# Performance work log

Hardware: AMD Instinct MI355X
Metric: run time of the kernel (lower is better)

## Reference

```python
import jax, jax.numpy as jnp
import numpy as np

N = 2000   # nodes
K = 16     # receptive-field size (exact degree incl. self-loop)
C_IN = 16  # input_feats
H = 16     # hidden_size
NC = 18    # num_contractions


def setup_inputs() -> dict:
    key = jax.random.key(0)
    k1, k2, k3, k4, k5, k6 = jax.random.split(key, 6)
    # adjacency with exactly K ones per row (self-loop + K-1 distinct random nbrs)
    u = jax.random.uniform(k1, (N, N))
    u = u.at[jnp.arange(N), jnp.arange(N)].set(-1.0)  # force self into top-K
    nbrs = jnp.argsort(u, axis=1)[:, :K]
    adj = jnp.zeros((N, N), jnp.float32).at[jnp.arange(N)[:, None], nbrs].set(1.0)
    X = jax.random.normal(k2, (N, C_IN), jnp.float32)
    scale = 0.1
    W1 = scale * jax.random.normal(k3, (H, NC * C_IN), jnp.float32)
    b1 = jnp.zeros((H,), jnp.float32)
    W2 = scale * jax.random.normal(k4, (H, NC * H), jnp.float32)
    b2 = jnp.zeros((H,), jnp.float32)
    fc_w = scale * jax.random.normal(k5, (1, 2 * H + C_IN), jnp.float32)
    fc_b = scale * jax.random.normal(k6, (1,), jnp.float32)
    return {"X": X, "adj": adj, "W1": W1, "b1": b1, "W2": W2, "b2": b2,
            "fc_w": fc_w, "fc_b": fc_b}


def _neighbors(adj):
    # each row has exactly K ones -> top_k returns their indices
    _, idx = jax.lax.top_k(adj, K)
    return jnp.sort(idx, axis=1)  # (N, K)


def _contract18(T):
    # T: (n, m, a, b, c) stacked promoted neighbor tensors; 18 contractions 3rd->2nd order
    n, k, _, _, c = T.shape
    tr = lambda M: jnp.swapaxes(M, 1, 2)
    s0, s1, s2 = T.sum(1), T.sum(2), T.sum(3)           # single-index sums
    d0 = jnp.einsum('ixxbc->ixbc', T)                    # diag m=a
    d1 = jnp.einsum('ixaxc->ixac', T)                    # diag m=b
    d2 = jnp.einsum('imyyc->imyc', T)                    # diag a=b
    outs = []
    for M in (s0, s1, s2, d0, d1, d2):
        outs.append(M)
        outs.append(tr(M))                               # 12 so far
    v0, v1, v2 = T.sum((2, 3)), T.sum((1, 3)), T.sum((1, 2))  # double sums -> vectors
    for v in (v0, v1, v2):
        outs.append(jnp.broadcast_to(v[:, :, None, :], (n, k, k, c)))  # rows
        outs.append(jnp.broadcast_to(v[:, None, :, :], (n, k, k, c)))  # cols
    return jnp.concatenate(outs, axis=-1)                # (n, k, k, 18c)


def _forward(X, adj, W1, b1, W2, b2, fc_w, fc_b):
    nbrs = _neighbors(adj)                               # (N, K)
    nbrs_nb = nbrs[nbrs]                                 # (N, K, K)
    # chi[i,m,a,b] = 1 iff a-th member of P_i equals b-th member of P_{nbrs[i,m]}
    chi = (nbrs[:, None, :, None] == nbrs_nb[:, :, None, :]).astype(X.dtype)  # (N,K,K,K)
    # F0: first->second order promotion (features on the diagonal of P_i x P_i)
    F0 = jnp.einsum('ab,iac->iabc', jnp.eye(K, dtype=X.dtype), X[nbrs])  # (N,K,K,C_IN)

    def step(F, W, b):
        Fn = F[nbrs]                                     # (N, m, p, q, c)
        tmp = jnp.einsum('imap,impqc->imaqc', chi, Fn)
        T = jnp.einsum('imaqc,imbq->imabc', tmp, chi)    # promoted + stacked (N,m,a,b,c)
        C = _contract18(T)                               # (N, a, b, 18c)
        return jax.nn.relu(jnp.einsum('iabk,hk->iabh', C, W) + b)

    F1 = step(F0, W1, b1)
    F2 = step(F1, W2, b2)
    g = jnp.concatenate([F0.sum((0, 1, 2)), F1.sum((0, 1, 2)), F2.sum((0, 1, 2))])
    return g @ fc_w.T + fc_b                             # (n_outputs,)


def reference(X, adj, W1, b1, W2, b2, fc_w, fc_b):
    return _forward(X, adj, W1, b1, W2, b2, fc_w, fc_b)
```

## Files before the change

### kernel.cpp

```cpp
#include <hip/hip_runtime.h>

#define NN 2000

typedef _Float16 halfx8 __attribute__((ext_vector_type(8)));
typedef float floatx4 __attribute__((ext_vector_type(4)));

#define LBAR() asm volatile("s_waitcnt lgkmcnt(0)\n\ts_barrier" ::: "memory")

__global__ void build_nbrs_k(const float* __restrict__ adj,
                             int* __restrict__ nbrs) {
    int i = blockIdx.x;
    int lane = threadIdx.x;
    const float* row = adj + (size_t)i * NN;
    float v[32];
#pragma unroll
    for (int c = 0; c < 32; ++c) {
        int col = c * 64 + lane;
        v[c] = (col < NN) ? row[col] : 0.0f;
    }
    int base = 0;
#pragma unroll
    for (int c = 0; c < 32; ++c) {
        bool p = v[c] > 0.5f;
        unsigned long long mask = __ballot(p);
        if (p) {
            int pos = base + __popcll(mask & ((1ull << lane) - 1ull));
            nbrs[i * 16 + pos] = c * 64 + lane;
        }
        base += __popcll(mask);
    }
}

__global__ void build_map_k(const int* __restrict__ nbrs,
                            signed char* __restrict__ map8,
                            signed char* __restrict__ imp8,
                            int4* __restrict__ aux) {
    int idx = blockIdx.x * blockDim.x + threadIdx.x;
    if (idx >= NN * 16) return;
    int i = idx >> 4;
    int m = idx & 15;
    int j = nbrs[idx];
    const int4* pi = (const int4*)(nbrs + (size_t)i * 16);
    const int4* pj = (const int4*)(nbrs + (size_t)j * 16);
    int4 A = pi[0], Bq = pi[1], C = pi[2], D = pi[3];
    int4 E = pj[0], F = pj[1], G = pj[2], H = pj[3];
    int ni[16] = {A.x,A.y,A.z,A.w, Bq.x,Bq.y,Bq.z,Bq.w, C.x,C.y,C.z,C.w, D.x,D.y,D.z,D.w};
    int nj[16] = {E.x,E.y,E.z,E.w, F.x,F.y,F.z,F.w, G.x,G.y,G.z,G.w, H.x,H.y,H.z,H.w};

    int mp[16];
    unsigned long long lo = 0, hi = 0;
#pragma unroll
    for (int a = 0; a < 16; ++a) {
        int r = -1;
#pragma unroll
        for (int p = 0; p < 16; ++p)
            if (nj[p] == ni[a]) r = p;
        mp[a] = r;
        unsigned long long b = (unsigned long long)(r & 0xff);
        if (a < 8) lo |= b << (8 * a); else hi |= b << (8 * (a - 8));
    }
    uint4 pk;
    pk.x = (unsigned)lo; pk.y = (unsigned)(lo >> 32);
    pk.z = (unsigned)hi; pk.w = (unsigned)(hi >> 32);
    *(uint4*)(map8 + ((size_t)idx << 4)) = pk;
    lo = 0; hi = 0;
#pragma unroll
    for (int p = 0; p < 16; ++p) {
        int r = -1;
#pragma unroll
        for (int a = 0; a < 16; ++a)
            if (ni[a] == nj[p]) r = a;
        unsigned long long b = (unsigned long long)(r & 0xff);
        if (p < 8) lo |= b << (8 * p); else hi |= b << (8 * (p - 8));
    }
    pk.x = (unsigned)lo; pk.y = (unsigned)(lo >> 32);
    pk.z = (unsigned)hi; pk.w = (unsigned)(hi >> 32);
    *(uint4*)(imp8 + ((size_t)idx << 4)) = pk;

    unsigned vm = 0;
    int a1 = -1, a2 = -1, pa1 = 0, pa2 = 0;
#pragma unroll
    for (int a = 0; a < 16; ++a) {
        if (mp[a] >= 0) {
            vm |= (1u << a);
            if (a1 < 0)      { a1 = a; pa1 = mp[a]; }
            else if (a2 < 0) { a2 = a; pa2 = mp[a]; }
        }
    }
    int ms = 0;
#pragma unroll
    for (int a = 0; a < 16; ++a)
        if (ni[a] == i) ms = a;
    int4 av;
    av.x = j;
    av.y = (a1 & 0xff) | ((pa1 & 0xff) << 8) | ((a2 & 0xff) << 16) | ((pa2 & 0xff) << 24);
    av.z = (int)(vm | ((unsigned)(mp[m] & 0xff) << 16) | ((unsigned)(ms & 0xff) << 24));
    av.w = 0;
    aux[idx] = av;
}

__global__ void prep_w_k(const float* __restrict__ W1,
                         const float* __restrict__ W2,
                         _Float16* __restrict__ Wpk) {
    int idx = blockIdx.x * blockDim.x + threadIdx.x;
    if (idx >= 2 * 10 * 512) return;
    int stage = idx / 5120;
    int rem = idx % 5120;
    int chunk = rem / 512;
    int r2 = rem % 512;
    int L = r2 / 8, jj = r2 % 8;
    int q = L >> 4, h = L & 15;
    int k = q * 8 + jj;
    const int tA[10] = {2, 6, 10, 0, 14,   3, 7, 11, 1, 15};
    const int tB[10] = {4, 8, -1, 12, 16,  5, 9, -1, 13, 17};
    int tblk = (k < 16) ? tA[chunk] : tB[chunk];
    int c = k & 15;
    const float* W = stage ? W2 : W1;
    float val = (tblk < 0) ? 0.f : W[h * 288 + tblk * 16 + c];
    Wpk[idx] = (_Float16)val;
}

template <int DIAG>
__global__ __launch_bounds__(256, 2)
void step_k(const float* __restrict__ Fp,
            const float* __restrict__ Xp,
            const _Float16* __restrict__ Wpk,
            const float* __restrict__ bias,
            const signed char* __restrict__ map8,
            const signed char* __restrict__ imp8,
            const int4* __restrict__ auxp,
            float* __restrict__ Fout,
            float* __restrict__ gp0,
            float* __restrict__ gp) {
    __shared__ __attribute__((aligned(16))) float S0[16][16][18];
    __shared__ __attribute__((aligned(16))) _Float16 MAP[5][16][16][16];
    __shared__ __attribute__((aligned(16))) float V0f[16][16];
    __shared__ __attribute__((aligned(16))) float V1f[16][16];
    __shared__ __attribute__((aligned(16))) float V2f[16][16];
    __shared__ __attribute__((aligned(16))) float S1f[16][16];

    const int i = blockIdx.x;
    const int t = threadIdx.x;
    const int u = t >> 4;
    const int l = t & 15;
    const int lane = t & 63, q = lane >> 4, h = lane & 15, wv = t >> 6;

    int4 av = auxp[i * 16 + u];
    uint4 imv = *(const uint4*)(imp8 + ((size_t)(i * 16 + u) << 4));
    float bv = bias[l];
    const int j = av.x;
    const int a1 = (int)(signed char)(av.y & 0xff);
    const int pa1 = (av.y >> 8) & 0xff;
    const int a2 = (int)(signed char)((av.y >> 16) & 0xff);
    const int pa2 = (av.y >> 24) & 0xff;
    const unsigned vm = (unsigned)(av.z & 0xffff);
    const int pmm = (av.z >> 16) & 0xff;
    const int ms = (av.z >> 24) & 0xff;

    float frow[16], fcol[16], xv = 0.f;
    if (DIAG) {
        xv = Xp[(size_t)j * 16 + l];
    } else {
        const float* Fi = Fp + (size_t)i * 4096;
#pragma unroll
        for (int b = 0; b < 16; ++b) frow[b] = Fi[(u * 16 + b) * 16 + l];
#pragma unroll
        for (int a = 0; a < 16; ++a) fcol[a] = Fi[(a * 16 + u) * 16 + l];
    }

    float R1[16], R2[16];
    if (!DIAG && u != ms) {
        const float* P1 = Fp + (((size_t)j * 256 + pa1 * 16) * 16) + l;
#pragma unroll
        for (int p = 0; p < 16; ++p) R1[p] = P1[p * 16];
        if (a2 >= 0) {
            const float* P2 = Fp + (((size_t)j * 256 + pa2 * 16) * 16) + l;
#pragma unroll
            for (int p = 0; p < 16; ++p) R2[p] = P2[p * 16];
        }
    }
    halfx8 Bf[10];
    {
        const halfx8* Wp8 = (const halfx8*)Wpk;
#pragma unroll
        for (int c = 0; c < 10; ++c) Bf[c] = Wp8[c * 64 + lane];
    }

    if (u != ms) {
        uint4 z = {0u, 0u, 0u, 0u};
#pragma unroll
        for (int k = 0; k < 5; ++k) {
            *(uint4*)&MAP[k][u][l][0] = z;
            *(uint4*)&MAP[k][u][l][8] = z;
        }
    }
    if (DIAG) {
        S1f[u][l] = xv;
        V1f[u][l] = xv;
        V2f[u][l] = xv;
#pragma unroll
        for (int b = 0; b < 16; ++b) S0[u][b][l] = (b == u) ? xv : 0.f;
        MAP[0][ms][u][l] = (_Float16)xv;
        MAP[1][ms][u][l] = (_Float16)xv;
        _Float16 dz = (_Float16)((u == ms) ? xv : 0.f);
        MAP[2][ms][u][l] = dz;
        MAP[3][ms][u][l] = dz;
        MAP[4][ms][u][l] = (_Float16)xv;
    } else {
        float s2 = 0.f, a10 = 0.f, a8 = 0.f;
#pragma unroll
        for (int b = 0; b < 16; ++b) {
            float v = frow[b];
            s2 += v;
            S0[u][b][l] = v;
            if (b == u)  a10 = v;
            if (b == ms) a8 = v;
        }
        float s1 = 0.f, a6 = 0.f;
#pragma unroll
        for (int a = 0; a < 16; ++a) {
            float v = fcol[a];
            s1 += v;
            if (a == ms) a6 = v;
        }
        S1f[u][l] = s2;
        V1f[u][l] = s2;
        V2f[u][l] = s1;
        MAP[0][ms][u][l] = (_Float16)s1;
        MAP[1][ms][u][l] = (_Float16)s2;
        MAP[2][ms][u][l] = (_Float16)a6;
        MAP[3][ms][u][l] = (_Float16)a8;
        MAP[4][ms][u][l] = (_Float16)a10;
    }
    LBAR();

    if (u != ms) {
        const int m = u;
        float v0acc = 0.f;
        if (DIAG) {
#pragma unroll
            for (int a = 0; a < 16; ++a) {
                if ((vm >> a) & 1u) {
                    float v = S1f[a][l];
                    v0acc += v;
                    atomicAdd(&S0[a][a][l], v);
                    atomicAdd(&V1f[a][l], v);
                    atomicAdd(&V2f[a][l], v);
                    MAP[0][m][a][l] = (_Float16)v;
                    MAP[1][m][a][l] = (_Float16)v;
                    MAP[4][m][a][l] = (_Float16)v;
                    if (a == m) { MAP[2][m][m][l] = (_Float16)v; MAP[3][m][m][l] = (_Float16)v; }
                }
            }
        } else {
            float colacc[16];
#pragma unroll
            for (int p = 0; p < 16; ++p) colacc[p] = 0.f;
            auto process = [&](int a, int pa, const float (&vr)[16]) {
                float rowacc = 0.f, a8v = 0.f, a10v = 0.f;
                const bool am = (a == m);
#pragma unroll
                for (int p = 0; p < 16; ++p) {
                    float v = vr[p];
                    if (p == pmm) a8v = v;
                    if (p == pa)  a10v = v;
                    unsigned dw = (p < 4) ? imv.x : ((p < 8) ? imv.y : ((p < 12) ? imv.z : imv.w));
                    int b = (int)(signed char)((dw >> (8 * (p & 3))) & 0xffu);
                    if (b >= 0) {
                        rowacc += v;
                        colacc[p] += v;
                        atomicAdd(&S0[a][b][l], v);
                        atomicAdd(&V2f[b][l], v);
                        if (am) MAP[2][m][b][l] = (_Float16)v;
                    }
                }
                v0acc += rowacc;
                atomicAdd(&V1f[a][l], rowacc);
                MAP[1][m][a][l] = (_Float16)rowacc;
                MAP[3][m][a][l] = (_Float16)a8v;
                MAP[4][m][a][l] = (_Float16)a10v;
            };
            process(a1, pa1, R1);
            if (a2 >= 0) process(a2, pa2, R2);
            unsigned rm = vm & ~(1u << a1);
            if (a2 >= 0) rm &= ~(1u << a2);
            if (rm) {
                uint4 mpq = *(const uint4*)(map8 + ((size_t)(i * 16 + u) << 4));
                do {
                    int a = __builtin_ctz(rm); rm &= rm - 1;
                    unsigned dw = (a & 8) ? ((a & 4) ? mpq.w : mpq.z) : ((a & 4) ? mpq.y : mpq.x);
                    int pa = (int)(signed char)((dw >> (8 * (a & 3))) & 0xffu);
                    float RT[16];
                    const float* P3 = Fp + (((size_t)j * 256 + pa * 16) * 16) + l;
#pragma unroll
                    for (int p = 0; p < 16; ++p) RT[p] = P3[p * 16];
                    process(a, pa, RT);
                } while (rm);
            }
#pragma unroll
            for (int p = 0; p < 16; ++p) {
                unsigned dw = (p < 4) ? imv.x : ((p < 8) ? imv.y : ((p < 12) ? imv.z : imv.w));
                int b = (int)(signed char)((dw >> (8 * (p & 3))) & 0xffu);
                if (b >= 0) MAP[0][m][b][l] = (_Float16)colacc[p];
            }
        }
        V0f[m][l] = v0acc;
    } else {
        float v0s = 0.f;
#pragma unroll
        for (int b = 0; b < 16; ++b) v0s += S1f[b][l];
        V0f[ms][l] = v0s;
        if (DIAG) gp0[l * 2048 + i] = v0s;
    }

    floatx4 acc1[4], acc2[4];
#pragma unroll
    for (int tt = 0; tt < 4; ++tt) {
        acc1[tt] = (floatx4){0.f, 0.f, 0.f, 0.f};
        acc2[tt] = (floatx4){0.f, 0.f, 0.f, 0.f};
    }
    halfx8 az;
#pragma unroll
    for (int z = 0; z < 8; ++z) az[z] = (_Float16)0.f;
    const int wbase = wv * 4;
#pragma unroll
    for (int tt = 0; tt < 4; ++tt) {
        const int x = wbase + tt;
        halfx8 p0, p1, p2;
        if (q < 2) {
            p0 = *(const halfx8*)&MAP[0][x][h][q * 8];
            p1 = *(const halfx8*)&MAP[2][x][h][q * 8];
            p2 = *(const halfx8*)&MAP[4][x][h][q * 8];
        } else {
            const int c0 = (q - 2) * 8;
            p0 = *(const halfx8*)&MAP[1][x][h][c0];
            p1 = *(const halfx8*)&MAP[3][x][h][c0];
            p2 = az;
        }
        acc1[tt] = __builtin_amdgcn_mfma_f32_16x16x32_f16(p0, Bf[0], acc1[tt], 0, 0, 0);
        acc1[tt] = __builtin_amdgcn_mfma_f32_16x16x32_f16(p1, Bf[1], acc1[tt], 0, 0, 0);
        acc1[tt] = __builtin_amdgcn_mfma_f32_16x16x32_f16(p2, Bf[2], acc1[tt], 0, 0, 0);
        acc2[tt] = __builtin_amdgcn_mfma_f32_16x16x32_f16(p0, Bf[5], acc2[tt], 0, 0, 0);
        acc2[tt] = __builtin_amdgcn_mfma_f32_16x16x32_f16(p1, Bf[6], acc2[tt], 0, 0, 0);
        acc2[tt] = __builtin_amdgcn_mfma_f32_16x16x32_f16(p2, Bf[7], acc2[tt], 0, 0, 0);
    }
    LBAR();

    auto cvt8 = [](const float* p) -> halfx8 {
        float2 fa = *(const float2*)p, fb = *(const float2*)(p + 2),
               fc = *(const float2*)(p + 4), fd = *(const float2*)(p + 6);
        halfx8 r;
        r[0] = (_Float16)fa.x; r[1] = (_Float16)fa.y; r[2] = (_Float16)fb.x; r[3] = (_Float16)fb.y;
        r[4] = (_Float16)fc.x; r[5] = (_Float16)fc.y; r[6] = (_Float16)fd.x; r[7] = (_Float16)fd.y;
        return r;
    };
    auto cvt8a = [](const float* p) -> halfx8 {
        float4 va = *(const float4*)p, vb = *(const float4*)(p + 4);
        halfx8 r;
        r[0] = (_Float16)va.x; r[1] = (_Float16)va.y; r[2] = (_Float16)va.z; r[3] = (_Float16)va.w;
        r[4] = (_Float16)vb.x; r[5] = (_Float16)vb.y; r[6] = (_Float16)vb.z; r[7] = (_Float16)vb.w;
        return r;
    };
#pragma unroll
    for (int tt = 0; tt < 4; ++tt) {
        const int x = wbase + tt;
        halfx8 p3, p4;
        if (q < 2) {
            p3 = cvt8(&S0[x][h][q * 8]);
            p4 = cvt8a(&V1f[x][q * 8]);
        } else {
            const int c0 = (q - 2) * 8;
            p3 = cvt8a(&V0f[x][c0]);
            p4 = cvt8a(&V2f[x][c0]);
        }
        acc1[tt] = __builtin_amdgcn_mfma_f32_16x16x32_f16(p3, Bf[3], acc1[tt], 0, 0, 0);
        acc1[tt] = __builtin_amdgcn_mfma_f32_16x16x32_f16(p4, Bf[4], acc1[tt], 0, 0, 0);
        acc2[tt] = __builtin_amdgcn_mfma_f32_16x16x32_f16(p3, Bf[8], acc2[tt], 0, 0, 0);
        acc2[tt] = __builtin_amdgcn_mfma_f32_16x16x32_f16(p4, Bf[9], acc2[tt], 0, 0, 0);
    }

    float* P2f = (float*)&MAP[0][0][0][0];
#pragma unroll
    for (int tt = 0; tt < 4; ++tt) {
        const int x = wbase + tt;
#pragma unroll
        for (int r = 0; r < 4; ++r)
            P2f[(x * 16 + (q * 4 + r)) * 17 + h] = acc2[tt][r];
    }
    LBAR();

    float gpart = 0.f;
#pragma unroll
    for (int tt = 0; tt < 4; ++tt) {
        const int x = wbase + tt;
#pragma unroll
        for (int r = 0; r < 4; ++r) {
            const int y = q * 4 + r;
            float val = acc1[tt][r] + P2f[(y * 16 + x) * 17 + h] + bv;
            val = fmaxf(val, 0.f);
            gpart += val;
            if (Fout) Fout[(size_t)i * 4096 + (x * 16 + y) * 16 + h] = val;
        }
    }
    gpart += __shfl_xor(gpart, 16, 64);
    gpart += __shfl_xor(gpart, 32, 64);
    if (lane < 16) gp[h * 8192 + i * 4 + wv] = gpart;
}

__global__ void reduce_g_k(const float* __restrict__ parts,
                           float* __restrict__ gsum) {
    int r = blockIdx.x;
    const float* p;
    int cnt4;
    if (r < 16)      { p = parts + r * 2048;                    cnt4 = 500;  }
    else if (r < 32) { p = parts + 32768 + (r - 16) * 8192;     cnt4 = 2000; }
    else             { p = parts + 163840 + (r - 32) * 8192;    cnt4 = 2000; }
    const float4* p4 = (const float4*)p;
    int t = threadIdx.x;
    float s = 0.f;
    for (int n = t; n < cnt4; n += 256) {
        float4 v = p4[n];
        s += v.x + v.y + v.z + v.w;
    }
#pragma unroll
    for (int off = 32; off > 0; off >>= 1) s += __shfl_xor(s, off, 64);
    __shared__ float wsum[4];
    if ((t & 63) == 0) wsum[t >> 6] = s;
    __syncthreads();
    if (t == 0) gsum[r] = wsum[0] + wsum[1] + wsum[2] + wsum[3];
}

__global__ void finalize_k(const float* __restrict__ gsum,
                           const float* __restrict__ fcw,
                           const float* __restrict__ fcb,
                           float* __restrict__ out) {
    int t = threadIdx.x;
    float v = (t < 48) ? gsum[t] * fcw[t] : 0.f;
#pragma unroll
    for (int off = 32; off > 0; off >>= 1) v += __shfl_xor(v, off, 64);
    if (t == 0) out[0] = v + fcb[0];
}

extern "C" void kernel_launch(void* const* d_in, const int* in_sizes, int n_in,
                              void* d_out, int out_size, void* d_ws, size_t ws_size,
                              hipStream_t stream) {
    const float* X   = (const float*)d_in[0];
    const float* adj = (const float*)d_in[1];
    const float* W1  = (const float*)d_in[2];
    const float* b1  = (const float*)d_in[3];
    const float* W2  = (const float*)d_in[4];
    const float* b2  = (const float*)d_in[5];
    const float* fcw = (const float*)d_in[6];
    const float* fcb = (const float*)d_in[7];
    float* out = (float*)d_out;
    char* ws = (char*)d_ws;

    float*       gsum  = (float*)(ws + 0);
    int*         nbrs  = (int*)(ws + 1024);
    signed char* map8  = (signed char*)(ws + 129280);
    signed char* imp8  = (signed char*)(ws + 641280);
    int4*        aux   = (int4*)(ws + 1153280);
    float*       parts = (float*)(ws + 1665280);
    _Float16*    Wpk   = (_Float16*)(ws + 2844928);
    float*       F1    = (float*)(ws + 2865408);

    build_nbrs_k<<<NN, 64, 0, stream>>>(adj, nbrs);
    build_map_k<<<(NN * 16 + 255) / 256, 256, 0, stream>>>(nbrs, map8, imp8, aux);
    prep_w_k<<<40, 256, 0, stream>>>(W1, W2, Wpk);
    step_k<1><<<NN, 256, 0, stream>>>(nullptr, X, Wpk, b1, map8, imp8, aux, F1,
                                      parts, parts + 32768);
    step_k<0><<<NN, 256, 0, stream>>>(F1, X, Wpk + 5120, b2, map8, imp8, aux, nullptr,
                                      nullptr, parts + 163840);
    reduce_g_k<<<48, 256, 0, stream>>>(parts, gsum);
    finalize_k<<<1, 64, 0, stream>>>(gsum, fcw, fcb, out);
}
```

Measured before the change: 158.1 us.

## Store MAP contraction tiles in FP8 and use FP8 MFMA for them

The five MAP contraction planes are now stored in shared memory as FP8 bytes, and the matching weight chunks are packed as FP8. The first group of matmuls uses fp8 MFMA instructions, while the S0/V-vector path stays in FP16. This halves the LDS footprint of MAP and drops the S0 padding, so launch bounds can rise from 2 to 4 blocks per CU for more occupancy. The cost is reduced precision on those contraction terms, plus extra conversion instructions, and possibly more LDS bank conflicts from the unpadded S0 atomics.

```diff
diff --git a/kernel.cpp b/kernel.cpp
--- a/kernel.cpp
+++ b/kernel.cpp
@@ -6,6 +6,10 @@
 typedef float floatx4 __attribute__((ext_vector_type(4)));
 
 #define LBAR() asm volatile("s_waitcnt lgkmcnt(0)\n\ts_barrier" ::: "memory")
+
+__device__ __forceinline__ unsigned char to_fp8(float v) {
+    return (unsigned char)(__builtin_amdgcn_cvt_pk_fp8_f32(v, 0.f, 0, false) & 0xff);
+}
 
 __global__ void build_nbrs_k(const float* __restrict__ adj,
                              int* __restrict__ nbrs) {
@@ -101,30 +105,50 @@
 
 __global__ void prep_w_k(const float* __restrict__ W1,
                          const float* __restrict__ W2,
-                         _Float16* __restrict__ Wpk) {
+                         unsigned char* __restrict__ Wpk8,
+                         _Float16* __restrict__ Wpk16) {
     int idx = blockIdx.x * blockDim.x + threadIdx.x;
-    if (idx >= 2 * 10 * 512) return;
-    int stage = idx / 5120;
-    int rem = idx % 5120;
-    int chunk = rem / 512;
-    int r2 = rem % 512;
-    int L = r2 / 8, jj = r2 % 8;
-    int q = L >> 4, h = L & 15;
-    int k = q * 8 + jj;
-    const int tA[10] = {2, 6, 10, 0, 14,   3, 7, 11, 1, 15};
-    const int tB[10] = {4, 8, -1, 12, 16,  5, 9, -1, 13, 17};
-    int tblk = (k < 16) ? tA[chunk] : tB[chunk];
-    int c = k & 15;
-    const float* W = stage ? W2 : W1;
-    float val = (tblk < 0) ? 0.f : W[h * 288 + tblk * 16 + c];
-    Wpk[idx] = (_Float16)val;
+    if (idx >= 10240) return;
+    if (idx < 6144) {
+        int stage = idx / 3072;
+        int r = idx % 3072;
+        int c = r / 512;
+        int r2 = r % 512;
+        int L = r2 >> 3, jj = r2 & 7;
+        int q = L >> 4, h = L & 15;
+        int k = q * 8 + jj;
+        const int bA[6] = {2, 6, 10, 3, 7, 11};
+        const int bB[6] = {4, 8, -1, 5, 9, -1};
+        int tb = (k < 16) ? bA[c] : bB[c];
+        int ci = k & 15;
+        const float* W = stage ? W2 : W1;
+        float val = (tb < 0) ? 0.f : W[h * 288 + tb * 16 + ci];
+        Wpk8[idx] = to_fp8(val);
+    } else {
+        int id2 = idx - 6144;
+        int stage = id2 / 2048;
+        int r = id2 % 2048;
+        int c = r / 512;
+        int r2 = r % 512;
+        int L = r2 >> 3, jj = r2 & 7;
+        int q = L >> 4, h = L & 15;
+        int k = q * 8 + jj;
+        const int bA[4] = {0, 14, 1, 15};
+        const int bB[4] = {12, 16, 13, 17};
+        int tb = (k < 16) ? bA[c] : bB[c];
+        int ci = k & 15;
+        const float* W = stage ? W2 : W1;
+        float val = W[h * 288 + tb * 16 + ci];
+        Wpk16[id2] = (_Float16)val;
+    }
 }
 
 template <int DIAG>
-__global__ __launch_bounds__(256, 2)
+__global__ __launch_bounds__(256, 4)
 void step_k(const float* __restrict__ Fp,
             const float* __restrict__ Xp,
-            const _Float16* __restrict__ Wpk,
+            const unsigned char* __restrict__ Wpk8s,
+            const _Float16* __restrict__ Wpk16s,
             const float* __restrict__ bias,
             const signed char* __restrict__ map8,
             const signed char* __restrict__ imp8,
@@ -132,8 +156,8 @@
             float* __restrict__ Fout,
             float* __restrict__ gp0,
             float* __restrict__ gp) {
-    __shared__ __attribute__((aligned(16))) float S0[16][16][18];
-    __shared__ __attribute__((aligned(16))) _Float16 MAP[5][16][16][16];
+    __shared__ __attribute__((aligned(16))) float S0[16][16][16];
+    __shared__ __attribute__((aligned(16))) unsigned char MAP8[5][16][16][16];
     __shared__ __attribute__((aligned(16))) float V0f[16][16];
     __shared__ __attribute__((aligned(16))) float V1f[16][16];
     __shared__ __attribute__((aligned(16))) float V2f[16][16];
@@ -179,20 +203,24 @@
             for (int p = 0; p < 16; ++p) R2[p] = P2[p * 16];
         }
     }
-    halfx8 Bf[10];
+    long Bf8[6];
     {
-        const halfx8* Wp8 = (const halfx8*)Wpk;
-#pragma unroll
-        for (int c = 0; c < 10; ++c) Bf[c] = Wp8[c * 64 + lane];
+        const long* Wq8 = (const long*)Wpk8s;
+#pragma unroll
+        for (int c = 0; c < 6; ++c) Bf8[c] = Wq8[c * 64 + lane];
+    }
+    halfx8 Bf16[4];
+    {
+        const halfx8* Wq16 = (const halfx8*)Wpk16s;
+#pragma unroll
+        for (int c = 0; c < 4; ++c) Bf16[c] = Wq16[c * 64 + lane];
     }
 
     if (u != ms) {
         uint4 z = {0u, 0u, 0u, 0u};
 #pragma unroll
-        for (int k = 0; k < 5; ++k) {
-            *(uint4*)&MAP[k][u][l][0] = z;
-            *(uint4*)&MAP[k][u][l][8] = z;
-        }
+        for (int k = 0; k < 5; ++k)
+            *(uint4*)&MAP8[k][u][l][0] = z;
     }
     if (DIAG) {
         S1f[u][l] = xv;
@@ -200,12 +228,13 @@
         V2f[u][l] = xv;
 #pragma unroll
         for (int b = 0; b < 16; ++b) S0[u][b][l] = (b == u) ? xv : 0.f;
-        MAP[0][ms][u][l] = (_Float16)xv;
-        MAP[1][ms][u][l] = (_Float16)xv;
-        _Float16 dz = (_Float16)((u == ms) ? xv : 0.f);
-        MAP[2][ms][u][l] = dz;
-        MAP[3][ms][u][l] = dz;
-        MAP[4][ms][u][l] = (_Float16)xv;
+        unsigned char x8 = to_fp8(xv);
+        MAP8[0][ms][u][l] = x8;
+        MAP8[1][ms][u][l] = x8;
+        unsigned char dz = (u == ms) ? x8 : (unsigned char)0;
+        MAP8[2][ms][u][l] = dz;
+        MAP8[3][ms][u][l] = dz;
+        MAP8[4][ms][u][l] = x8;
     } else {
         float s2 = 0.f, a10 = 0.f, a8 = 0.f;
 #pragma unroll
@@ -226,11 +255,11 @@
         S1f[u][l] = s2;
         V1f[u][l] = s2;
         V2f[u][l] = s1;
-        MAP[0][ms][u][l] = (_Float16)s1;
-        MAP[1][ms][u][l] = (_Float16)s2;
-        MAP[2][ms][u][l] = (_Float16)a6;
-        MAP[3][ms][u][l] = (_Float16)a8;
-        MAP[4][ms][u][l] = (_Float16)a10;
+        MAP8[0][ms][u][l] = to_fp8(s1);
+        MAP8[1][ms][u][l] = to_fp8(s2);
+        MAP8[2][ms][u][l] = to_fp8(a6);
+        MAP8[3][ms][u][l] = to_fp8(a8);
+        MAP8[4][ms][u][l] = to_fp8(a10);
     }
     LBAR();
 
@@ -246,10 +275,11 @@
                     atomicAdd(&S0[a][a][l], v);
                     atomicAdd(&V1f[a][l], v);
                     atomicAdd(&V2f[a][l], v);
-                    MAP[0][m][a][l] = (_Float16)v;
-                    MAP[1][m][a][l] = (_Float16)v;
-                    MAP[4][m][a][l] = (_Float16)v;
-                    if (a == m) { MAP[2][m][m][l] = (_Float16)v; MAP[3][m][m][l] = (_Float16)v; }
+                    unsigned char v8 = to_fp8(v);
+                    MAP8[0][m][a][l] = v8;
+                    MAP8[1][m][a][l] = v8;
+                    MAP8[4][m][a][l] = v8;
+                    if (a == m) { MAP8[2][m][m][l] = v8; MAP8[3][m][m][l] = v8; }
                 }
             }
         } else {
@@ -271,14 +301,14 @@
                         colacc[p] += v;
                         atomicAdd(&S0[a][b][l], v);
                         atomicAdd(&V2f[b][l], v);
-                        if (am) MAP[2][m][b][l] = (_Float16)v;
+                        if (am) MAP8[2][m][b][l] = to_fp8(v);
                     }
                 }
                 v0acc += rowacc;
                 atomicAdd(&V1f[a][l], rowacc);
-                MAP[1][m][a][l] = (_Float16)rowacc;
-                MAP[3][m][a][l] = (_Float16)a8v;
-                MAP[4][m][a][l] = (_Float16)a10v;
+                MAP8[1][m][a][l] = to_fp8(rowacc);
+                MAP8[3][m][a][l] = to_fp8(a8v);
+                MAP8[4][m][a][l] = to_fp8(a10v);
             };
             process(a1, pa1, R1);
             if (a2 >= 0) process(a2, pa2, R2);
@@ -301,7 +331,7 @@
             for (int p = 0; p < 16; ++p) {
                 unsigned dw = (p < 4) ? imv.x : ((p < 8) ? imv.y : ((p < 12) ? imv.z : imv.w));
                 int b = (int)(signed char)((dw >> (8 * (p & 3))) & 0xffu);
-                if (b >= 0) MAP[0][m][b][l] = (_Float16)colacc[p];
+                if (b >= 0) MAP8[0][m][b][l] = to_fp8(colacc[p]);
             }
         }
         V0f[m][l] = v0acc;
@@ -319,41 +349,29 @@
         acc1[tt] = (floatx4){0.f, 0.f, 0.f, 0.f};
         acc2[tt] = (floatx4){0.f, 0.f, 0.f, 0.f};
     }
-    halfx8 az;
-#pragma unroll
-    for (int z = 0; z < 8; ++z) az[z] = (_Float16)0.f;
     const int wbase = wv * 4;
-#pragma unroll
-    for (int tt = 0; tt < 4; ++tt) {
-        const int x = wbase + tt;
-        halfx8 p0, p1, p2;
-        if (q < 2) {
-            p0 = *(const halfx8*)&MAP[0][x][h][q * 8];
-            p1 = *(const halfx8*)&MAP[2][x][h][q * 8];
-            p2 = *(const halfx8*)&MAP[4][x][h][q * 8];
-        } else {
-            const int c0 = (q - 2) * 8;
-            p0 = *(const halfx8*)&MAP[1][x][h][c0];
-            p1 = *(const halfx8*)&MAP[3][x][h][c0];
-            p2 = az;
-        }
-        acc1[tt] = __builtin_amdgcn_mfma_f32_16x16x32_f16(p0, Bf[0], acc1[tt], 0, 0, 0);
-        acc1[tt] = __builtin_amdgcn_mfma_f32_16x16x32_f16(p1, Bf[1], acc1[tt], 0, 0, 0);
-        acc1[tt] = __builtin_amdgcn_mfma_f32_16x16x32_f16(p2, Bf[2], acc1[tt], 0, 0, 0);
-        acc2[tt] = __builtin_amdgcn_mfma_f32_16x16x32_f16(p0, Bf[5], acc2[tt], 0, 0, 0);
-        acc2[tt] = __builtin_amdgcn_mfma_f32_16x16x32_f16(p1, Bf[6], acc2[tt], 0, 0, 0);
-        acc2[tt] = __builtin_amdgcn_mfma_f32_16x16x32_f16(p2, Bf[7], acc2[tt], 0, 0, 0);
+    {
+        const int off8 = (q & 1) * 8;
+        const unsigned char* mA = (q < 2) ? &MAP8[0][0][0][0] : &MAP8[1][0][0][0];
+        const unsigned char* mB = (q < 2) ? &MAP8[2][0][0][0] : &MAP8[3][0][0][0];
+        const unsigned char* mC = &MAP8[4][0][0][0];
+#pragma unroll
+        for (int tt = 0; tt < 4; ++tt) {
+            const int x = wbase + tt;
+            const int base = x * 256 + h * 16 + off8;
+            long f0 = *(const long*)(mA + base);
+            long f1 = *(const long*)(mB + base);
+            long f2 = (q < 2) ? *(const long*)(mC + base) : 0L;
+            acc1[tt] = __builtin_amdgcn_mfma_f32_16x16x32_fp8_fp8(f0, Bf8[0], acc1[tt], 0, 0, 0);
+            acc1[tt] = __builtin_amdgcn_mfma_f32_16x16x32_fp8_fp8(f1, Bf8[1], acc1[tt], 0, 0, 0);
+            acc1[tt] = __builtin_amdgcn_mfma_f32_16x16x32_fp8_fp8(f2, Bf8[2], acc1[tt], 0, 0, 0);
+            acc2[tt] = __builtin_amdgcn_mfma_f32_16x16x32_fp8_fp8(f0, Bf8[3], acc2[tt], 0, 0, 0);
+            acc2[tt] = __builtin_amdgcn_mfma_f32_16x16x32_fp8_fp8(f1, Bf8[4], acc2[tt], 0, 0, 0);
+            acc2[tt] = __builtin_amdgcn_mfma_f32_16x16x32_fp8_fp8(f2, Bf8[5], acc2[tt], 0, 0, 0);
+        }
     }
     LBAR();
 
-    auto cvt8 = [](const float* p) -> halfx8 {
-        float2 fa = *(const float2*)p, fb = *(const float2*)(p + 2),
-               fc = *(const float2*)(p + 4), fd = *(const float2*)(p + 6);
-        halfx8 r;
-        r[0] = (_Float16)fa.x; r[1] = (_Float16)fa.y; r[2] = (_Float16)fb.x; r[3] = (_Float16)fb.y;
-        r[4] = (_Float16)fc.x; r[5] = (_Float16)fc.y; r[6] = (_Float16)fd.x; r[7] = (_Float16)fd.y;
-        return r;
-    };
     auto cvt8a = [](const float* p) -> halfx8 {
         float4 va = *(const float4*)p, vb = *(const float4*)(p + 4);
         halfx8 r;
@@ -366,20 +384,20 @@
         const int x = wbase + tt;
         halfx8 p3, p4;
         if (q < 2) {
-            p3 = cvt8(&S0[x][h][q * 8]);
+            p3 = cvt8a(&S0[x][h][q * 8]);
             p4 = cvt8a(&V1f[x][q * 8]);
         } else {
             const int c0 = (q - 2) * 8;
             p3 = cvt8a(&V0f[x][c0]);
             p4 = cvt8a(&V2f[x][c0]);
         }
-        acc1[tt] = __builtin_amdgcn_mfma_f32_16x16x32_f16(p3, Bf[3], acc1[tt], 0, 0, 0);
-        acc1[tt] = __builtin_amdgcn_mfma_f32_16x16x32_f16(p4, Bf[4], acc1[tt], 0, 0, 0);
-        acc2[tt] = __builtin_amdgcn_mfma_f32_16x16x32_f16(p3, Bf[8], acc2[tt], 0, 0, 0);
-        acc2[tt] = __builtin_amdgcn_mfma_f32_16x16x32_f16(p4, Bf[9], acc2[tt], 0, 0, 0);
-    }
-
-    float* P2f = (float*)&MAP[0][0][0][0];
+        acc1[tt] = __builtin_amdgcn_mfma_f32_16x16x32_f16(p3, Bf16[0], acc1[tt], 0, 0, 0);
+        acc1[tt] = __builtin_amdgcn_mfma_f32_16x16x32_f16(p4, Bf16[1], acc1[tt], 0, 0, 0);
+        acc2[tt] = __builtin_amdgcn_mfma_f32_16x16x32_f16(p3, Bf16[2], acc2[tt], 0, 0, 0);
+        acc2[tt] = __builtin_amdgcn_mfma_f32_16x16x32_f16(p4, Bf16[3], acc2[tt], 0, 0, 0);
+    }
+
+    float* P2f = (float*)&MAP8[0][0][0][0];
 #pragma unroll
     for (int tt = 0; tt < 4; ++tt) {
         const int x = wbase + tt;
@@ -455,22 +473,23 @@
     float* out = (float*)d_out;
     char* ws = (char*)d_ws;
 
-    float*       gsum  = (float*)(ws + 0);
-    int*         nbrs  = (int*)(ws + 1024);
-    signed char* map8  = (signed char*)(ws + 129280);
-    signed char* imp8  = (signed char*)(ws + 641280);
-    int4*        aux   = (int4*)(ws + 1153280);
-    float*       parts = (float*)(ws + 1665280);
-    _Float16*    Wpk   = (_Float16*)(ws + 2844928);
-    float*       F1    = (float*)(ws + 2865408);
+    float*         gsum  = (float*)(ws + 0);
+    int*           nbrs  = (int*)(ws + 1024);
+    signed char*   map8  = (signed char*)(ws + 129280);
+    signed char*   imp8  = (signed char*)(ws + 641280);
+    int4*          aux   = (int4*)(ws + 1153280);
+    float*         parts = (float*)(ws + 1665280);
+    unsigned char* Wpk8  = (unsigned char*)(ws + 2844928);
+    _Float16*      Wpk16 = (_Float16*)(ws + 2851072);
+    float*         F1    = (float*)(ws + 2859264);
 
     build_nbrs_k<<<NN, 64, 0, stream>>>(adj, nbrs);
     build_map_k<<<(NN * 16 + 255) / 256, 256, 0, stream>>>(nbrs, map8, imp8, aux);
-    prep_w_k<<<40, 256, 0, stream>>>(W1, W2, Wpk);
-    step_k<1><<<NN, 256, 0, stream>>>(nullptr, X, Wpk, b1, map8, imp8, aux, F1,
+    prep_w_k<<<40, 256, 0, stream>>>(W1, W2, Wpk8, Wpk16);
+    step_k<1><<<NN, 256, 0, stream>>>(nullptr, X, Wpk8, Wpk16, b1, map8, imp8, aux, F1,
                                       parts, parts + 32768);
-    step_k<0><<<NN, 256, 0, stream>>>(F1, X, Wpk + 5120, b2, map8, imp8, aux, nullptr,
-                                      nullptr, parts + 163840);
+    step_k<0><<<NN, 256, 0, stream>>>(F1, X, Wpk8 + 3072, Wpk16 + 2048, b2, map8, imp8, aux,
+                                      nullptr, nullptr, parts + 163840);
     reduce_g_k<<<48, 256, 0, stream>>>(parts, gsum);
     finalize_k<<<1, 64, 0, stream>>>(gsum, fcw, fcb, out);
 }
```

Result: slower. 172.3 us (+9.0%).
